# Performance work log

Measured on AMD Instinct MI355X. Metric: run time of the kernel, lower is better.

The kernel has to match this reference:

```python
import jax, jax.numpy as jnp
import numpy as np

D_MODEL = 96
EXPAND = 2.0
D_INNER = int(EXPAND * D_MODEL)  # 192
D_STATE = 1
DT_RANK = 6  # ceil(96/16)
K = 4
B, H, W = 4, 128, 128
L = H * W


def setup_inputs() -> dict:
    key = jax.random.key(0)
    ks = jax.random.split(key, 12)
    x = jax.random.normal(ks[0], (B, D_MODEL, H, W), dtype=jnp.float32)
    # 4 per-direction scan permutations of L and their inverses
    scan_ids = jnp.stack([jax.random.permutation(jax.random.fold_in(ks[1], k), L) for k in range(K)]).astype(jnp.int32)
    inverse_ids = jnp.argsort(scan_ids, axis=1).astype(jnp.int32)
    in_proj_w = jax.random.normal(ks[2], (D_INNER, D_MODEL), dtype=jnp.float32) * (1.0 / np.sqrt(D_MODEL))
    conv_w = jax.random.normal(ks[3], (D_INNER, 1, 3, 3), dtype=jnp.float32) * (1.0 / 3.0)
    conv_b = jax.random.normal(ks[4], (D_INNER,), dtype=jnp.float32) * 0.02
    x_proj_weight = jax.random.normal(ks[5], (K, DT_RANK + 2 * D_STATE, D_INNER), dtype=jnp.float32) * (1.0 / np.sqrt(D_INNER))
    dt_projs_weight = 0.1 * jax.random.uniform(ks[6], (K, D_INNER, DT_RANK), dtype=jnp.float32)
    dt_projs_bias = 0.1 * jax.random.uniform(ks[7], (K, D_INNER), dtype=jnp.float32)
    A_logs = jnp.zeros((K * D_INNER, D_STATE), dtype=jnp.float32)
    Ds = jnp.ones((K * D_INNER,), dtype=jnp.float32)
    out_proj_w = jax.random.normal(ks[8], (D_MODEL, D_INNER), dtype=jnp.float32) * (1.0 / np.sqrt(D_INNER))
    return {"x": x, "scan_ids": scan_ids, "inverse_ids": inverse_ids,
            "in_proj_w": in_proj_w, "conv_w": conv_w, "conv_b": conv_b,
            "x_proj_weight": x_proj_weight, "dt_projs_weight": dt_projs_weight,
            "dt_projs_bias": dt_projs_bias, "A_logs": A_logs, "Ds": Ds,
            "out_proj_w": out_proj_w}


def _selective_scan(u, delta, A, Bs, Cs, Ds, delta_bias):
    # u, delta: (B,K,D,L); A: (K,D,N); Bs, Cs: (B,K,N,L); Ds: (K,D); delta_bias: (K,D)
    delta = jax.nn.softplus(delta + delta_bias[None, :, :, None])  # (B,K,D,L)
    a = jnp.exp(delta[:, :, :, None, :] * A[None, :, :, :, None])  # (B,K,D,N,L)
    bu = delta[:, :, :, None, :] * Bs[:, :, None, :, :] * u[:, :, :, None, :]  # (B,K,D,N,L)

    def combine(lhs, rhs):
        aL, bL = lhs
        aR, bR = rhs
        return aR * aL, aR * bL + bR

    _, h = jax.lax.associative_scan(combine, (a, bu), axis=-1)  # h: (B,K,D,N,L)
    y = jnp.einsum('bknl,bkdnl->bkdl', Cs, h) + Ds[None, :, :, None] * u
    return y


def reference(x, scan_ids, inverse_ids, in_proj_w, conv_w, conv_b, x_proj_weight,
              dt_projs_weight, dt_projs_bias, A_logs, Ds, out_proj_w):
    Bsz, _, Hh, Ww = x.shape
    Ll = Hh * Ww
    # in_proj (1x1 conv == linear over channels)
    x = jnp.einsum('oc,bchw->bohw', in_proj_w, x)
    # depthwise 3x3 conv, padding SAME
    x = jax.lax.conv_general_dilated(x, conv_w, (1, 1), 'SAME',
                                     dimension_numbers=('NCHW', 'OIHW', 'NCHW'),
                                     feature_group_count=D_INNER)
    x = x + conv_b[None, :, None, None]
    x = jax.nn.silu(x)
    # 4-direction gather: (B,D,L) -> (B,K,D,L)
    xf = x.reshape(Bsz, D_INNER, Ll)
    xs = jnp.transpose(xf[:, :, scan_ids], (0, 2, 1, 3))  # (B,K,D,L)
    # input-dependent projections
    x_dbl = jnp.einsum('bkdl,kcd->bkcl', xs, x_proj_weight)
    dts, Bm, Cm = jnp.split(x_dbl, [DT_RANK, DT_RANK + D_STATE], axis=2)
    dts = jnp.einsum('bkrl,kdr->bkdl', dts, dt_projs_weight)
    A = -jnp.exp(A_logs.astype(jnp.float32)).reshape(K, D_INNER, D_STATE)
    ys = _selective_scan(xs.astype(jnp.float32), dts.astype(jnp.float32), A,
                         Bm.astype(jnp.float32), Cm.astype(jnp.float32),
                         Ds.astype(jnp.float32).reshape(K, D_INNER),
                         dt_projs_bias.astype(jnp.float32))  # (B,K,D,L)
    # inverse scatter per direction (gather with inverse permutation), then sum
    yinv = jnp.take_along_axis(ys, inverse_ids[None, :, None, :].astype(jnp.int32), axis=-1)
    y = jnp.sum(yinv, axis=1).reshape(Bsz, D_INNER, Hh, Ww)
    y = jax.nn.gelu(y)
    out = jnp.einsum('oc,bchw->bohw', out_proj_w, y)
    return out
```

## Files before the change

### kernel.cpp

```cpp
#include <hip/hip_runtime.h>
#include <math.h>

#define BATCH 4
#define HH 128
#define WWW 128
#define LLEN (HH*WWW)
#define CIN 96
#define DI 192
#define KDIR 4
#define NCH 512
#define PCH 32

__global__ __launch_bounds__(256) void k_inproj(const float* __restrict__ x,
                                                const float* __restrict__ w,
                                                float* __restrict__ t0) {
    __shared__ float xin[CIN * 64];
    __shared__ float wt[CIN * 65];
    int bid = blockIdx.x;
    int b = bid >> 8;
    int l0 = (bid & 255) << 6;
    int t = threadIdx.x;
    for (int i = 0; i < 24; ++i) {
        int idx = t + i * 256;
        int c = idx >> 6, l = idx & 63;
        xin[c * 64 + l] = x[((size_t)(b * CIN + c)) * LLEN + l0 + l];
    }
    int o_lane = t & 63;
    int lgrp = t >> 6;
    for (int ot = 0; ot < 3; ++ot) {
        __syncthreads();
        for (int i = 0; i < 24; ++i) {
            int idx = t + i * 256;
            int o = idx / 96, c = idx - o * 96;
            wt[c * 65 + o] = w[(ot * 64 + o) * 96 + c];
        }
        __syncthreads();
        float4 acc4[4];
        #pragma unroll
        for (int i = 0; i < 4; ++i) acc4[i] = make_float4(0.f, 0.f, 0.f, 0.f);
        int lb = lgrp * 16;
        for (int c = 0; c < CIN; ++c) {
            float wv = wt[c * 65 + o_lane];
            const float4* xv = reinterpret_cast<const float4*>(&xin[c * 64 + lb]);
            #pragma unroll
            for (int i = 0; i < 4; ++i) {
                float4 xx = xv[i];
                acc4[i].x += wv * xx.x; acc4[i].y += wv * xx.y;
                acc4[i].z += wv * xx.z; acc4[i].w += wv * xx.w;
            }
        }
        int o = ot * 64 + o_lane;
        #pragma unroll
        for (int i = 0; i < 4; ++i) {
            t0[((size_t)(b * LLEN) + l0 + lb + i * 4 + 0) * DI + o] = acc4[i].x;
            t0[((size_t)(b * LLEN) + l0 + lb + i * 4 + 1) * DI + o] = acc4[i].y;
            t0[((size_t)(b * LLEN) + l0 + lb + i * 4 + 2) * DI + o] = acc4[i].z;
            t0[((size_t)(b * LLEN) + l0 + lb + i * 4 + 3) * DI + o] = acc4[i].w;
        }
    }
}

__global__ __launch_bounds__(192) void k_dwconv(const float* __restrict__ t0,
                                                const float* __restrict__ cw,
                                                const float* __restrict__ cb,
                                                float* __restrict__ xf) {
    int bid = blockIdx.x;
    int wt = (bid & 15) << 3;
    int h  = (bid >> 4) & (HH - 1);
    int b  = bid >> 11;
    int d  = threadIdx.x;
    float acc[8];
    float bias = cb[d];
    #pragma unroll
    for (int j = 0; j < 8; ++j) acc[j] = bias;
    #pragma unroll
    for (int kh = 0; kh < 3; ++kh) {
        int hh = h + kh - 1;
        if (hh < 0 || hh >= HH) continue;
        float w0v = cw[d * 9 + kh * 3 + 0];
        float w1v = cw[d * 9 + kh * 3 + 1];
        float w2v = cw[d * 9 + kh * 3 + 2];
        const float* rowp = t0 + ((size_t)(b * LLEN) + hh * WWW) * DI + d;
        float v[10];
        #pragma unroll
        for (int j = 0; j < 10; ++j) {
            int ww = wt + j - 1;
            v[j] = (ww < 0 || ww >= WWW) ? 0.f : rowp[(size_t)ww * DI];
        }
        #pragma unroll
        for (int j = 0; j < 8; ++j)
            acc[j] += w0v * v[j] + w1v * v[j + 1] + w2v * v[j + 2];
    }
    size_t outbase = ((size_t)(b * LLEN) + h * WWW + wt) * DI + d;
    #pragma unroll
    for (int j = 0; j < 8; ++j) {
        float aa = acc[j];
        float s = aa * __builtin_amdgcn_rcpf(1.f + __expf(-aa));
        xf[outbase + (size_t)j * DI] = s;
    }
}

__global__ __launch_bounds__(256) void k_scan1(const float* __restrict__ xf,
                                               const int* __restrict__ sids,
                                               const float* __restrict__ xpw,
                                               const float* __restrict__ dtw,
                                               const float* __restrict__ dtb,
                                               const float* __restrict__ alog,
                                               const float* __restrict__ dsv,
                                               float* __restrict__ cA,
                                               float* __restrict__ cB,
                                               float* __restrict__ xdblg) {
    __shared__ float xs[DI * 33];
    __shared__ float part[32 * 4 * 9];
    __shared__ float xdbl[PCH * 8];
    __shared__ int sid[PCH];
    int bid = blockIdx.x;
    int c = bid & (NCH - 1);
    int k = (bid >> 9) & 3;
    int b = bid >> 11;
    int t = threadIdx.x;
    if (t < PCH) sid[t] = sids[k * LLEN + c * PCH + t];
    __syncthreads();
    {
        int p = t & 31, s = t >> 5;
        const float* row = xf + ((size_t)(b * LLEN) + sid[p]) * DI + s * 24;
        float4 v[6];
        #pragma unroll
        for (int j = 0; j < 6; ++j) v[j] = reinterpret_cast<const float4*>(row)[j];
        #pragma unroll
        for (int j = 0; j < 6; ++j) {
            int d0 = s * 24 + j * 4;
            xs[(d0 + 0) * 33 + p] = v[j].x;
            xs[(d0 + 1) * 33 + p] = v[j].y;
            xs[(d0 + 2) * 33 + p] = v[j].z;
            xs[(d0 + 3) * 33 + p] = v[j].w;
        }
        const float* wbase = xpw + (size_t)k * 8 * DI + s * 24;
        float pd[8];
        #pragma unroll
        for (int co = 0; co < 8; ++co) {
            const float4* w4 = reinterpret_cast<const float4*>(wbase + co * DI);
            float a0 = 0.f;
            #pragma unroll
            for (int j = 0; j < 6; ++j) {
                float4 wv = w4[j];
                a0 += wv.x * v[j].x + wv.y * v[j].y + wv.z * v[j].z + wv.w * v[j].w;
            }
            pd[co] = a0;
        }
        #pragma unroll
        for (int co = 0; co < 8; ++co) pd[co] += __shfl_xor(pd[co], 32);
        if ((s & 1) == 0) {
            int wq = s >> 1;
            #pragma unroll
            for (int co = 0; co < 8; ++co) part[(p * 4 + wq) * 9 + co] = pd[co];
        }
    }
    __syncthreads();
    {
        int p = t >> 3, co = t & 7;
        float s = part[(p * 4 + 0) * 9 + co] + part[(p * 4 + 1) * 9 + co] +
                  part[(p * 4 + 2) * 9 + co] + part[(p * 4 + 3) * 9 + co];
        xdbl[p * 8 + co] = s;
        xdblg[(size_t)bid * (PCH * 8) + t] = s;
    }
    __syncthreads();
    if (t < DI) {
        int d = t;
        float wr[6];
        #pragma unroll
        for (int r = 0; r < 6; ++r) wr[r] = dtw[(k * DI + d) * 6 + r];
        float bias = dtb[k * DI + d];
        float A = -__expf(alog[k * DI + d]);
        float Ar = 1.f, Br = 0.f;
        const float4* xd4 = reinterpret_cast<const float4*>(xdbl);
        #pragma unroll
        for (int p = 0; p < PCH; ++p) {
            float4 x0 = xd4[p * 2], x1 = xd4[p * 2 + 1];
            float s = bias + wr[0] * x0.x + wr[1] * x0.y + wr[2] * x0.z +
                      wr[3] * x0.w + wr[4] * x1.x + wr[5] * x1.y;
            float delta = (s > 20.f) ? s : __logf(1.f + __expf(s));
            float a = __expf(delta * A);
            float bu = delta * x1.z * xs[d * 33 + p];
            Br = a * Br + bu;
            Ar *= a;
        }
        cA[(size_t)bid * DI + d] = Ar;
        cB[(size_t)bid * DI + d] = Br;
    }
}

__global__ __launch_bounds__(192) void k_cs1(const float* __restrict__ cA,
                                             const float* __restrict__ cB,
                                             float* __restrict__ segA,
                                             float* __restrict__ segB) {
    int g = blockIdx.x;
    int d = threadIdx.x;
    size_t base = (size_t)g * 32 * DI + d;
    float A = 1.f, Bv = 0.f;
    for (int cc = 0; cc < 32; ++cc) {
        float a = cA[base + (size_t)cc * DI];
        float bb = cB[base + (size_t)cc * DI];
        Bv = a * Bv + bb;
        A *= a;
    }
    segA[(size_t)g * DI + d] = A;
    segB[(size_t)g * DI + d] = Bv;
}
__global__ __launch_bounds__(192) void k_cs2(const float* __restrict__ segA,
                                             const float* __restrict__ segB,
                                             float* __restrict__ hseg) {
    int bk = blockIdx.x;
    int d = threadIdx.x;
    float h = 0.f;
    for (int seg = 0; seg < 16; ++seg) {
        size_t idx = (size_t)(bk * 16 + seg) * DI + d;
        hseg[idx] = h;
        h = segA[idx] * h + segB[idx];
    }
}
__global__ __launch_bounds__(192) void k_cs3(const float* __restrict__ cA,
                                             float* __restrict__ cB,
                                             const float* __restrict__ hseg) {
    int g = blockIdx.x;
    int d = threadIdx.x;
    float h = hseg[(size_t)g * DI + d];
    size_t base = (size_t)g * 32 * DI + d;
    for (int cc = 0; cc < 32; ++cc) {
        size_t ix = base + (size_t)cc * DI;
        float a = cA[ix];
        float bb = cB[ix];
        cB[ix] = h;
        h = a * h + bb;
    }
}

template <bool ACCUM>
__global__ __launch_bounds__(192) void k_scan3(const float* __restrict__ xf,
                                               const int* __restrict__ sids,
                                               const float* __restrict__ dtw,
                                               const float* __restrict__ dtb,
                                               const float* __restrict__ alog,
                                               const float* __restrict__ dsv,
                                               const float* __restrict__ hin,
                                               const float* __restrict__ xdblg,
                                               float* __restrict__ y,
                                               int k) {
    __shared__ float xdbl[PCH * 8];
    __shared__ int sid[PCH];
    int bid = blockIdx.x;
    int c = bid & (NCH - 1);
    int b = bid >> 9;
    int t = threadIdx.x;
    size_t gidx = (size_t)((b * KDIR + k) * NCH + c);
    if (t < PCH) sid[t] = sids[k * LLEN + c * PCH + t];
    if (t < 64) {
        reinterpret_cast<float4*>(xdbl)[t] =
            reinterpret_cast<const float4*>(xdblg + gidx * (PCH * 8))[t];
    }
    __syncthreads();
    int d = t;
    const float* ubase = xf + (size_t)(b * LLEN) * DI + d;
    float* ybase = y + (size_t)(b * LLEN) * DI + d;
    float uv[PCH];
    #pragma unroll
    for (int p = 0; p < PCH; ++p) uv[p] = ubase[(size_t)sid[p] * DI];
    float yv[PCH];
    if (ACCUM) {
        #pragma unroll
        for (int p = 0; p < PCH; ++p) yv[p] = ybase[(size_t)sid[p] * DI];
    }
    float wr[6];
    #pragma unroll
    for (int r = 0; r < 6; ++r) wr[r] = dtw[(k * DI + d) * 6 + r];
    float bias = dtb[k * DI + d];
    float A = -__expf(alog[k * DI + d]);
    float Dv = dsv[k * DI + d];
    float h = hin[gidx * DI + d];
    const float4* xd4 = reinterpret_cast<const float4*>(xdbl);
    #pragma unroll
    for (int p = 0; p < PCH; ++p) {
        float4 x0 = xd4[p * 2], x1 = xd4[p * 2 + 1];
        float s = bias + wr[0] * x0.x + wr[1] * x0.y + wr[2] * x0.z +
                  wr[3] * x0.w + wr[4] * x1.x + wr[5] * x1.y;
        float delta = (s > 20.f) ? s : __logf(1.f + __expf(s));
        float a = __expf(delta * A);
        float bu = delta * x1.z * uv[p];
        h = a * h + bu;
        float ys = x1.w * h + Dv * uv[p];
        if (ACCUM) ys += yv[p];
        ybase[(size_t)sid[p] * DI] = ys;
    }
}

__global__ __launch_bounds__(256) void k_out(const float* __restrict__ y,
                                             const float* __restrict__ wo,
                                             float* __restrict__ out) {
    __shared__ float gy[DI * 65];
    int bid = blockIdx.x;
    int b = bid >> 8;
    int l0 = (bid & 255) << 6;
    int t = threadIdx.x;
    for (int i = 0; i < 48; ++i) {
        int idx = t + i * 256;
        int l = idx / DI;
        int cc = idx - l * DI;
        float v = y[((size_t)(b * LLEN) + l0 + l) * DI + cc];
        float z = 0.7978845608028654f * (v + 0.044715f * v * v * v);
        float e = __expf(2.f * z);
        float th = 1.f - 2.f * __builtin_amdgcn_rcpf(e + 1.f);
        gy[cc * 65 + l] = 0.5f * v * (1.f + th);
    }
    __syncthreads();
    int lq = t & 15, oh = t >> 4;
    float acc[6][4];
    #pragma unroll
    for (int i = 0; i < 6; ++i)
        #pragma unroll
        for (int e = 0; e < 4; ++e) acc[i][e] = 0.f;
    for (int cc = 0; cc < DI; cc += 4) {
        float4 wv[6];
        #pragma unroll
        for (int i = 0; i < 6; ++i)
            wv[i] = *reinterpret_cast<const float4*>(&wo[(oh * 6 + i) * DI + cc]);
        float g[4][4];
        #pragma unroll
        for (int el = 0; el < 4; ++el) {
            g[el][0] = gy[(cc + 0) * 65 + lq * 4 + el];
            g[el][1] = gy[(cc + 1) * 65 + lq * 4 + el];
            g[el][2] = gy[(cc + 2) * 65 + lq * 4 + el];
            g[el][3] = gy[(cc + 3) * 65 + lq * 4 + el];
        }
        #pragma unroll
        for (int i = 0; i < 6; ++i)
            #pragma unroll
            for (int el = 0; el < 4; ++el)
                acc[i][el] += wv[i].x * g[el][0] + wv[i].y * g[el][1] +
                              wv[i].z * g[el][2] + wv[i].w * g[el][3];
    }
    #pragma unroll
    for (int i = 0; i < 6; ++i) {
        int o = oh * 6 + i;
        float4 st = make_float4(acc[i][0], acc[i][1], acc[i][2], acc[i][3]);
        *reinterpret_cast<float4*>(&out[((size_t)(b * CIN) + o) * LLEN + l0 + lq * 4]) = st;
    }
}

extern "C" void kernel_launch(void* const* d_in, const int* in_sizes, int n_in,
                              void* d_out, int out_size, void* d_ws, size_t ws_size,
                              hipStream_t stream) {
    const float* x        = (const float*)d_in[0];
    const int*   scan_ids = (const int*)d_in[1];
    const float* in_proj_w = (const float*)d_in[3];
    const float* conv_w    = (const float*)d_in[4];
    const float* conv_b    = (const float*)d_in[5];
    const float* xpw       = (const float*)d_in[6];
    const float* dtw       = (const float*)d_in[7];
    const float* dtb       = (const float*)d_in[8];
    const float* alog      = (const float*)d_in[9];
    const float* dsv       = (const float*)d_in[10];
    const float* wo        = (const float*)d_in[11];
    float* out = (float*)d_out;

    float* ws = (float*)d_ws;
    const size_t NBL  = (size_t)BATCH * LLEN * DI;
    const size_t NCK  = (size_t)BATCH * KDIR * NCH * DI;
    const size_t NXD  = (size_t)BATCH * KDIR * LLEN * 8;
    const size_t NSG  = (size_t)BATCH * KDIR * 16 * DI;
    float* t0    = ws;
    float* xf    = t0 + NBL;
    float* xdblg = xf + NBL;
    float* cA    = xdblg + NXD;
    float* cB    = cA + NCK;
    float* segA  = cB + NCK;
    float* segB  = segA + NSG;
    float* hseg  = segB + NSG;
    float* y     = t0;

    k_inproj<<<BATCH * 256, 256, 0, stream>>>(x, in_proj_w, t0);
    k_dwconv<<<BATCH * HH * 16, 192, 0, stream>>>(t0, conv_w, conv_b, xf);
    k_scan1<<<BATCH * KDIR * NCH, 256, 0, stream>>>(xf, scan_ids, xpw, dtw, dtb,
                                                    alog, dsv, cA, cB, xdblg);
    k_cs1<<<BATCH * KDIR * 16, 192, 0, stream>>>(cA, cB, segA, segB);
    k_cs2<<<BATCH * KDIR, 192, 0, stream>>>(segA, segB, hseg);
    k_cs3<<<BATCH * KDIR * 16, 192, 0, stream>>>(cA, cB, hseg);
    k_scan3<false><<<BATCH * NCH, 192, 0, stream>>>(xf, scan_ids, dtw, dtb,
                                                    alog, dsv, cB, xdblg, y, 0);
    for (int k = 1; k < KDIR; ++k)
        k_scan3<true><<<BATCH * NCH, 192, 0, stream>>>(xf, scan_ids, dtw, dtb,
                                                       alog, dsv, cB, xdblg, y, k);
    k_out<<<BATCH * 256, 256, 0, stream>>>(y, wo, out);
}
```

Measured before the change: 442.0 us.

## Compute x_proj for all four directions once in original order before scans

Adds a k_proj kernel that computes the 32-channel x_proj output (8 per direction × 4) for each spatial position in natural order, with coalesced reads of xf and the weights staged in shared memory. Because x_proj is pointwise, it commutes with the permutation. The scan kernels then gather the per-position xdbl values through scan_ids instead of recomputing the projection from gathered rows. k_scan1 becomes a lighter 192-thread kernel that loads u per thread. The cost is an extra kernel launch and scattered 16-byte gathers of xdbl.

```diff
diff --git a/kernel.cpp b/kernel.cpp
--- a/kernel.cpp
+++ b/kernel.cpp
@@ -100,18 +100,66 @@
     }
 }
 
-__global__ __launch_bounds__(256) void k_scan1(const float* __restrict__ xf,
+__global__ __launch_bounds__(256) void k_proj(const float* __restrict__ xf,
+                                              const float* __restrict__ xpw,
+                                              float* __restrict__ xdblp) {
+    __shared__ float wl[32 * DI];
+    __shared__ float part[4 * 32 * 33];
+    int bid = blockIdx.x;
+    int t = threadIdx.x;
+    {
+        const float4* wsrc = reinterpret_cast<const float4*>(xpw);
+        float4* wdst = reinterpret_cast<float4*>(wl);
+        #pragma unroll
+        for (int i = 0; i < 6; ++i) wdst[t + i * 256] = wsrc[t + i * 256];
+    }
+    int p = t & 31, s = t >> 5;
+    const float4* row = reinterpret_cast<const float4*>(
+        xf + ((size_t)bid * 32 + p) * DI + s * 24);
+    float4 v[6];
+    #pragma unroll
+    for (int j = 0; j < 6; ++j) v[j] = row[j];
+    __syncthreads();
+    float pd[32];
+    #pragma unroll
+    for (int ch = 0; ch < 32; ++ch) {
+        const float4* w4 = reinterpret_cast<const float4*>(wl + ch * DI + s * 24);
+        float a0 = 0.f;
+        #pragma unroll
+        for (int j = 0; j < 6; ++j) {
+            float4 wv = w4[j];
+            a0 += wv.x * v[j].x + wv.y * v[j].y + wv.z * v[j].z + wv.w * v[j].w;
+        }
+        pd[ch] = a0;
+    }
+    #pragma unroll
+    for (int ch = 0; ch < 32; ++ch) pd[ch] += __shfl_xor(pd[ch], 32);
+    if ((s & 1) == 0) {
+        int wq = s >> 1;
+        #pragma unroll
+        for (int ch = 0; ch < 32; ++ch) part[(wq * 32 + p) * 33 + ch] = pd[ch];
+    }
+    __syncthreads();
+    int pos = t >> 3, c4 = t & 7;
+    float r[4];
+    #pragma unroll
+    for (int i = 0; i < 4; ++i) {
+        int ch = c4 * 4 + i;
+        r[i] = part[pos * 33 + ch] + part[(32 + pos) * 33 + ch] +
+               part[(64 + pos) * 33 + ch] + part[(96 + pos) * 33 + ch];
+    }
+    reinterpret_cast<float4*>(xdblp + (size_t)bid * 1024)[t] =
+        make_float4(r[0], r[1], r[2], r[3]);
+}
+
+__global__ __launch_bounds__(192) void k_scan1(const float* __restrict__ xf,
                                                const int* __restrict__ sids,
-                                               const float* __restrict__ xpw,
+                                               const float* __restrict__ xdblp,
                                                const float* __restrict__ dtw,
                                                const float* __restrict__ dtb,
                                                const float* __restrict__ alog,
-                                               const float* __restrict__ dsv,
                                                float* __restrict__ cA,
-                                               float* __restrict__ cB,
-                                               float* __restrict__ xdblg) {
-    __shared__ float xs[DI * 33];
-    __shared__ float part[32 * 4 * 9];
+                                               float* __restrict__ cB) {
     __shared__ float xdbl[PCH * 8];
     __shared__ int sid[PCH];
     int bid = blockIdx.x;
@@ -121,73 +169,37 @@
     int t = threadIdx.x;
     if (t < PCH) sid[t] = sids[k * LLEN + c * PCH + t];
     __syncthreads();
-    {
-        int p = t & 31, s = t >> 5;
-        const float* row = xf + ((size_t)(b * LLEN) + sid[p]) * DI + s * 24;
-        float4 v[6];
-        #pragma unroll
-        for (int j = 0; j < 6; ++j) v[j] = reinterpret_cast<const float4*>(row)[j];
-        #pragma unroll
-        for (int j = 0; j < 6; ++j) {
-            int d0 = s * 24 + j * 4;
-            xs[(d0 + 0) * 33 + p] = v[j].x;
-            xs[(d0 + 1) * 33 + p] = v[j].y;
-            xs[(d0 + 2) * 33 + p] = v[j].z;
-            xs[(d0 + 3) * 33 + p] = v[j].w;
-        }
-        const float* wbase = xpw + (size_t)k * 8 * DI + s * 24;
-        float pd[8];
-        #pragma unroll
-        for (int co = 0; co < 8; ++co) {
-            const float4* w4 = reinterpret_cast<const float4*>(wbase + co * DI);
-            float a0 = 0.f;
-            #pragma unroll
-            for (int j = 0; j < 6; ++j) {
-                float4 wv = w4[j];
-                a0 += wv.x * v[j].x + wv.y * v[j].y + wv.z * v[j].z + wv.w * v[j].w;
-            }
-            pd[co] = a0;
-        }
-        #pragma unroll
-        for (int co = 0; co < 8; ++co) pd[co] += __shfl_xor(pd[co], 32);
-        if ((s & 1) == 0) {
-            int wq = s >> 1;
-            #pragma unroll
-            for (int co = 0; co < 8; ++co) part[(p * 4 + wq) * 9 + co] = pd[co];
-        }
-    }
-    __syncthreads();
-    {
-        int p = t >> 3, co = t & 7;
-        float s = part[(p * 4 + 0) * 9 + co] + part[(p * 4 + 1) * 9 + co] +
-                  part[(p * 4 + 2) * 9 + co] + part[(p * 4 + 3) * 9 + co];
-        xdbl[p * 8 + co] = s;
-        xdblg[(size_t)bid * (PCH * 8) + t] = s;
-    }
-    __syncthreads();
-    if (t < DI) {
-        int d = t;
-        float wr[6];
-        #pragma unroll
-        for (int r = 0; r < 6; ++r) wr[r] = dtw[(k * DI + d) * 6 + r];
-        float bias = dtb[k * DI + d];
-        float A = -__expf(alog[k * DI + d]);
-        float Ar = 1.f, Br = 0.f;
-        const float4* xd4 = reinterpret_cast<const float4*>(xdbl);
-        #pragma unroll
-        for (int p = 0; p < PCH; ++p) {
-            float4 x0 = xd4[p * 2], x1 = xd4[p * 2 + 1];
-            float s = bias + wr[0] * x0.x + wr[1] * x0.y + wr[2] * x0.z +
-                      wr[3] * x0.w + wr[4] * x1.x + wr[5] * x1.y;
-            float delta = (s > 20.f) ? s : __logf(1.f + __expf(s));
-            float a = __expf(delta * A);
-            float bu = delta * x1.z * xs[d * 33 + p];
-            Br = a * Br + bu;
-            Ar *= a;
-        }
-        cA[(size_t)bid * DI + d] = Ar;
-        cB[(size_t)bid * DI + d] = Br;
-    }
+    if (t < 64) {
+        int p = t >> 1, half = t & 1;
+        reinterpret_cast<float4*>(xdbl)[t] = *reinterpret_cast<const float4*>(
+            xdblp + ((size_t)(b * LLEN) + sid[p]) * 32 + k * 8 + half * 4);
+    }
+    __syncthreads();
+    int d = t;
+    const float* ubase = xf + (size_t)(b * LLEN) * DI + d;
+    float uv[PCH];
+    #pragma unroll
+    for (int p = 0; p < PCH; ++p) uv[p] = ubase[(size_t)sid[p] * DI];
+    float wr[6];
+    #pragma unroll
+    for (int r = 0; r < 6; ++r) wr[r] = dtw[(k * DI + d) * 6 + r];
+    float bias = dtb[k * DI + d];
+    float A = -__expf(alog[k * DI + d]);
+    float Ar = 1.f, Br = 0.f;
+    const float4* xd4 = reinterpret_cast<const float4*>(xdbl);
+    #pragma unroll
+    for (int p = 0; p < PCH; ++p) {
+        float4 x0 = xd4[p * 2], x1 = xd4[p * 2 + 1];
+        float s = bias + wr[0] * x0.x + wr[1] * x0.y + wr[2] * x0.z +
+                  wr[3] * x0.w + wr[4] * x1.x + wr[5] * x1.y;
+        float delta = (s > 20.f) ? s : __logf(1.f + __expf(s));
+        float a = __expf(delta * A);
+        float bu = delta * x1.z * uv[p];
+        Br = a * Br + bu;
+        Ar *= a;
+    }
+    cA[(size_t)bid * DI + d] = Ar;
+    cB[(size_t)bid * DI + d] = Br;
 }
 
 __global__ __launch_bounds__(192) void k_cs1(const float* __restrict__ cA,
@@ -243,7 +255,7 @@
                                                const float* __restrict__ alog,
                                                const float* __restrict__ dsv,
                                                const float* __restrict__ hin,
-                                               const float* __restrict__ xdblg,
+                                               const float* __restrict__ xdblp,
                                                float* __restrict__ y,
                                                int k) {
     __shared__ float xdbl[PCH * 8];
@@ -254,9 +266,11 @@
     int t = threadIdx.x;
     size_t gidx = (size_t)((b * KDIR + k) * NCH + c);
     if (t < PCH) sid[t] = sids[k * LLEN + c * PCH + t];
+    __syncthreads();
     if (t < 64) {
-        reinterpret_cast<float4*>(xdbl)[t] =
-            reinterpret_cast<const float4*>(xdblg + gidx * (PCH * 8))[t];
+        int p = t >> 1, half = t & 1;
+        reinterpret_cast<float4*>(xdbl)[t] = *reinterpret_cast<const float4*>(
+            xdblp + ((size_t)(b * LLEN) + sid[p]) * 32 + k * 8 + half * 4);
     }
     __syncthreads();
     int d = t;
@@ -365,12 +379,12 @@
     float* ws = (float*)d_ws;
     const size_t NBL  = (size_t)BATCH * LLEN * DI;
     const size_t NCK  = (size_t)BATCH * KDIR * NCH * DI;
-    const size_t NXD  = (size_t)BATCH * KDIR * LLEN * 8;
+    const size_t NXD  = (size_t)BATCH * LLEN * 32;
     const size_t NSG  = (size_t)BATCH * KDIR * 16 * DI;
     float* t0    = ws;
     float* xf    = t0 + NBL;
-    float* xdblg = xf + NBL;
-    float* cA    = xdblg + NXD;
+    float* xdblp = xf + NBL;
+    float* cA    = xdblp + NXD;
     float* cB    = cA + NCK;
     float* segA  = cB + NCK;
     float* segB  = segA + NSG;
@@ -379,15 +393,16 @@
 
     k_inproj<<<BATCH * 256, 256, 0, stream>>>(x, in_proj_w, t0);
     k_dwconv<<<BATCH * HH * 16, 192, 0, stream>>>(t0, conv_w, conv_b, xf);
-    k_scan1<<<BATCH * KDIR * NCH, 256, 0, stream>>>(xf, scan_ids, xpw, dtw, dtb,
-                                                    alog, dsv, cA, cB, xdblg);
+    k_proj<<<(BATCH * LLEN) / 32, 256, 0, stream>>>(xf, xpw, xdblp);
+    k_scan1<<<BATCH * KDIR * NCH, 192, 0, stream>>>(xf, scan_ids, xdblp, dtw, dtb,
+                                                    alog, cA, cB);
     k_cs1<<<BATCH * KDIR * 16, 192, 0, stream>>>(cA, cB, segA, segB);
     k_cs2<<<BATCH * KDIR, 192, 0, stream>>>(segA, segB, hseg);
     k_cs3<<<BATCH * KDIR * 16, 192, 0, stream>>>(cA, cB, hseg);
     k_scan3<false><<<BATCH * NCH, 192, 0, stream>>>(xf, scan_ids, dtw, dtb,
-                                                    alog, dsv, cB, xdblg, y, 0);
+                                                    alog, dsv, cB, xdblp, y, 0);
     for (int k = 1; k < KDIR; ++k)
         k_scan3<true><<<BATCH * NCH, 192, 0, stream>>>(xf, scan_ids, dtw, dtb,
-                                                       alog, dsv, cB, xdblg, y, k);
+                                                       alog, dsv, cB, xdblp, y, k);
     k_out<<<BATCH * 256, 256, 0, stream>>>(y, wo, out);
 }
```

New measurement: 433.1 us. 2.0% less time.
